# Performance work log

Hardware: AMD Instinct MI355X
Metric: run time of the kernel (lower is better)

## Reference

```python
import jax, jax.numpy as jnp
from jax import lax
import numpy as np

COMMITMENT_COST = 0.25
N_EMBED = 512
EDIM = 32


def _conv(x, w, b, stride, pad):
    # x: NCHW, w: OIHW (torch Conv2d layout)
    y = lax.conv_general_dilated(x, w, (stride, stride), [(pad, pad), (pad, pad)],
                                 dimension_numbers=("NCHW", "OIHW", "NCHW"))
    return y + b[None, :, None, None]


def _conv_t(x, w, b, stride, pad):
    # torch ConvTranspose2d weight layout: (in, out, kH, kW)
    k = w.shape[2]
    w_ = jnp.flip(w, (2, 3)).transpose(1, 0, 2, 3)  # -> OIHW
    p = k - 1 - pad
    y = lax.conv_general_dilated(x, w_, (1, 1), [(p, p), (p, p)],
                                 lhs_dilation=(stride, stride),
                                 dimension_numbers=("NCHW", "OIHW", "NCHW"))
    return y + b[None, :, None, None]


def setup_inputs() -> dict:
    key = jax.random.key(0)
    ks = jax.random.split(key, 9)
    rn = lambda k, s: jax.random.normal(k, s, jnp.float32) * 0.05
    return {
        "x": jax.random.normal(ks[0], (32, 3, 256, 256), jnp.float32),
        "e_w1": rn(ks[1], (64, 3, 4, 4)),    "e_b1": jnp.zeros((64,), jnp.float32),
        "e_w2": rn(ks[2], (128, 64, 4, 4)),  "e_b2": jnp.zeros((128,), jnp.float32),
        "e_w3": rn(ks[3], (32, 128, 3, 3)),  "e_b3": jnp.zeros((32,), jnp.float32),
        "embed": jax.random.uniform(ks[4], (N_EMBED, EDIM), jnp.float32,
                                    -1.0 / N_EMBED, 1.0 / N_EMBED),
        "d_w1": rn(ks[5], (32, 128, 3, 3)),  "d_b1": jnp.zeros((128,), jnp.float32),
        "d_w2": rn(ks[6], (128, 64, 4, 4)),  "d_b2": jnp.zeros((64,), jnp.float32),
        "d_w3": rn(ks[7], (64, 3, 4, 4)),    "d_b3": jnp.zeros((3,), jnp.float32),
    }


def reference(x, e_w1, e_b1, e_w2, e_b2, e_w3, e_b3, embed,
              d_w1, d_b1, d_w2, d_b2, d_w3, d_b3):
    # ---- encoder ----
    h = jax.nn.relu(_conv(x, e_w1, e_b1, 2, 1))   # [B,64,128,128]
    h = jax.nn.relu(_conv(h, e_w2, e_b2, 2, 1))   # [B,128,64,64]
    z = jax.nn.relu(_conv(h, e_w3, e_b3, 1, 1))   # [B,32,64,64]
    # ---- vector quantizer ----
    zp = z.transpose(0, 2, 3, 1)                  # BHWC
    zf = zp.reshape(-1, EDIM)                     # [N, 32]
    d = (zf ** 2).sum(1, keepdims=True) + (embed ** 2).sum(1) \
        - 2.0 * zf @ embed.T                      # [N, n_embed]
    idx = jnp.argmin(d, axis=1)                   # [N]
    z_q = embed[idx].reshape(zp.shape)            # gather == onehot @ embed
    sg = lax.stop_gradient
    loss = jnp.mean((sg(z_q) - zp) ** 2) + COMMITMENT_COST * jnp.mean((z_q - sg(zp)) ** 2)
    z_q_st = zp + sg(z_q - zp)                    # straight-through
    z_q_st = z_q_st.transpose(0, 3, 1, 2)         # back to NCHW
    # ---- decoder ----
    h = jax.nn.relu(_conv_t(z_q_st, d_w1, d_b1, 1, 1))  # [B,128,64,64]
    h = jax.nn.relu(_conv_t(h, d_w2, d_b2, 2, 1))       # [B,64,128,128]
    x_recon = _conv_t(h, d_w3, d_b3, 2, 1)              # [B,3,256,256]
    return x_recon, loss
```

## Files before the change

kernel.cpp:

```cpp
#include <hip/hip_runtime.h>


typedef __attribute__((ext_vector_type(8))) short     short8;
typedef __attribute__((ext_vector_type(4))) short     s16x4;
typedef __attribute__((ext_vector_type(8))) __bf16    bf16x8;
typedef __attribute__((ext_vector_type(4))) float     f32x4;
typedef __attribute__((ext_vector_type(4))) unsigned  uint32x4;

#define BATCH 32

__device__ __forceinline__ float b2f(unsigned short b) {
  union { unsigned u; float f; } v; v.u = ((unsigned)b) << 16; return v.f;
}
__device__ __forceinline__ unsigned short f2b(float f) {
  union { float f; unsigned u; } v; v.f = f;
  unsigned r = v.u + 0x7FFF + ((v.u >> 16) & 1);
  return (unsigned short)(r >> 16);
}

__global__ __launch_bounds__(256) void prep1v_k(const float* __restrict__ w,
                                                unsigned short* __restrict__ wq) {
  const int i = blockIdx.x*256 + threadIdx.x;
  const int j = i & 7, l = (i >> 3) & 63, ni = (i >> 9) & 3, ks = i >> 11;
  const int k = ks*32 + (l >> 4)*8 + j;
  const int co = ni*16 + (l & 15);
  wq[i] = (k < 48) ? f2b(w[co*48 + k]) : (unsigned short)0;
}
__global__ __launch_bounds__(256) void prep2v_k(const float* __restrict__ w,
                                                unsigned short* __restrict__ wq) {
  const int i = blockIdx.x*256 + threadIdx.x;
  const int j = i & 7, l = (i >> 3) & 63, ni = (i >> 9) & 7, ks = i >> 12;
  const int lm = l & 15, lk = l >> 4;
  const int tap = ks >> 1, cc = ks & 1;
  const int co = ni*16 + lm, ci = cc*32 + lk*8 + j;
  wq[i] = f2b(w[(co*64 + ci)*16 + tap]);
}
__global__ __launch_bounds__(256) void prep3_k(const float* __restrict__ w,
                                               unsigned short* __restrict__ wq) {
  const int i = blockIdx.x*256 + threadIdx.x;
  const int ci = i & 127, co = (i >> 7) & 31, t = i >> 12;
  wq[i] = f2b(w[(co*128 + ci)*9 + t]);
}
__global__ __launch_bounds__(256) void prep4_k(const float* __restrict__ w,
                                               unsigned short* __restrict__ wq) {
  const int i = blockIdx.x*256 + threadIdx.x;
  const int ci = i & 31, co = (i >> 5) & 127, t = i >> 12;
  wq[i] = f2b(w[(ci*128 + co)*9 + (8 - t)]);
}
__global__ __launch_bounds__(256) void prep5v_k(const float* __restrict__ w,
                                                unsigned short* __restrict__ wq) {
  const int i = blockIdx.x*256 + threadIdx.x;
  const int j = i & 7, l = (i >> 3) & 63, ni = (i >> 9) & 3;
  const int ks = (i >> 11) & 15, p = i >> 15;
  const int lm = l & 15, lk = l >> 4;
  const int py = p >> 1, px = p & 1;
  const int a = ks >> 3, b = (ks >> 2) & 1, cc = ks & 3;
  const int co = ni*16 + lm, ci = cc*32 + lk*8 + j;
  const int ky = 3 - 2*a - py, kx = 3 - 2*b - px;
  wq[i] = f2b(w[(ci*64 + co)*16 + ky*4 + kx]);
}
__global__ __launch_bounds__(256) void prep6_k(const float* __restrict__ w,
                                               unsigned short* __restrict__ wq) {
  const int i = blockIdx.x*256 + threadIdx.x;
  const int j = i & 7, l = (i >> 3) & 63, kc = (i >> 9) & 7, p = i >> 12;
  const int lm = l & 15, lk = l >> 4;
  const int a = kc >> 2, b = (kc >> 1) & 1, ch = kc & 1;
  const int ci = ch*32 + lk*8 + j, co = lm;
  const int py = p >> 1, px = p & 1;
  const int ky = 2 - 2*a + (1 - py), kx = 2 - 2*b + (1 - px);
  wq[i] = (co < 3) ? f2b(w[(ci*3 + co)*16 + ky*4 + kx]) : (unsigned short)0;
}

template<int CIN,int COUT,int HIN,int S,int KW,int NTAPS,int OSTRIDE,int P,
         bool PARITY,bool RELU,bool INF32,bool OUTF32>
__global__ __launch_bounds__(256) void mconv_k(const void* __restrict__ in_,
    const unsigned short* __restrict__ wq_, const float* __restrict__ bias,
    void* __restrict__ out_) {
  constexpr int NF  = COUT / 16;
  constexpr int NCH = CIN / 32;
  __shared__ short Al[128*40];
  __shared__ short Bl[COUT*40];
  int py = 0, px = 0, PY = P, PX = P;
  const unsigned short* wq = wq_;
  if (PARITY) {
    py = blockIdx.y >> 1; px = blockIdx.y & 1;
    PY = 1 - py; PX = 1 - px;
    wq += blockIdx.y * (NTAPS*COUT*CIN);
  }
  const int m0 = blockIdx.x * 128;
  const int w  = threadIdx.x >> 6, l = threadIdx.x & 63;
  const int lm = l & 15, lk = l >> 4;
  f32x4 acc[2][NF];
  #pragma unroll
  for (int mi = 0; mi < 2; ++mi)
    #pragma unroll
    for (int ni = 0; ni < NF; ++ni) acc[mi][ni] = (f32x4)0.0f;

  for (int tap = 0; tap < NTAPS; ++tap) {
    const int ky = tap / KW, kx = tap % KW;
    for (int ch = 0; ch < NCH; ++ch) {
      const int c0 = ch * 32;
      __syncthreads();
      for (int s = threadIdx.x; s < 512; s += 256) {
        const int row = s >> 2, part = s & 3;
        const int m = m0 + row;
        const int n = m >> 12, oy = (m >> 6) & 63, ox = m & 63;
        const int iy = oy*S - PY + ky, ix = ox*S - PX + kx;
        short8 v = (short8)(short)0;
        if (iy >= 0 && iy < HIN && ix >= 0 && ix < HIN) {
          const int base = ((n*HIN + iy)*HIN + ix)*CIN + c0 + part*8;
          if (INF32) {
            const float* pf = (const float*)in_ + base;
            const f32x4 f0 = *(const f32x4*)pf;
            const f32x4 f1 = *(const f32x4*)(pf + 4);
            #pragma unroll
            for (int j = 0; j < 4; ++j) {
              v[j]     = (short)f2b(f0[j]);
              v[j + 4] = (short)f2b(f1[j]);
            }
          } else {
            v = *(const short8*)((const unsigned short*)in_ + base);
          }
        }
        *(short8*)&Al[row*40 + part*8] = v;
      }
      for (int s = threadIdx.x; s < COUT*4; s += 256) {
        const int co = s >> 2, part = s & 3;
        *(short8*)&Bl[co*40 + part*8] =
            *(const short8*)(wq + (tap*COUT + co)*CIN + c0 + part*8);
      }
      __syncthreads();
      short8 av[2];
      #pragma unroll
      for (int mi = 0; mi < 2; ++mi)
        av[mi] = *(const short8*)&Al[(w*32 + mi*16 + lm)*40 + lk*8];
      #pragma unroll
      for (int ni = 0; ni < NF; ++ni) {
        const short8 bv = *(const short8*)&Bl[(ni*16 + lm)*40 + lk*8];
        #pragma unroll
        for (int mi = 0; mi < 2; ++mi)
          acc[mi][ni] = __builtin_amdgcn_mfma_f32_16x16x32_bf16(
              __builtin_bit_cast(bf16x8, av[mi]),
              __builtin_bit_cast(bf16x8, bv),
              acc[mi][ni], 0, 0, 0);
      }
    }
  }
  #pragma unroll
  for (int ni = 0; ni < NF; ++ni) {
    const int co = ni*16 + lm;
    const float bv = bias[co];
    #pragma unroll
    for (int mi = 0; mi < 2; ++mi) {
      #pragma unroll
      for (int r = 0; r < 4; ++r) {
        const int ml = w*32 + mi*16 + lk*4 + r;
        const int m  = m0 + ml;
        float vv = acc[mi][ni][r] + bv;
        if (RELU) vv = fmaxf(vv, 0.f);
        int off;
        if (OSTRIDE == 1) {
          off = m*COUT + co;
        } else {
          const int n = m >> 12, oy = (m >> 6) & 63, ox = m & 63;
          off = ((n*128 + oy*2 + py)*128 + ox*2 + px)*COUT + co;
        }
        if (OUTF32) ((float*)out_)[off] = vv;
        else ((unsigned short*)out_)[off] = f2b(vv);
      }
    }
  }
}

__global__ __launch_bounds__(256) void conv1m_k(const float* __restrict__ x,
    const unsigned short* __restrict__ wv, const float* __restrict__ bias,
    unsigned short* __restrict__ out) {
  __shared__ __align__(16) short RAW[12*264];
  __shared__ __align__(16) short IC[128*64];
  const int wid = ((blockIdx.x & 7) << 9) + (blockIdx.x >> 3);
  const int q = wid & 127, n = wid >> 7;
  for (int i = threadIdx.x; i < 396; i += 256)
    *(short8*)&RAW[i*8] = (short8)(short)0;
  __syncthreads();
  for (int s = threadIdx.x; s < 768; s += 256) {
    const int g = s >> 6, seg = s & 63;
    const int ci = g >> 2, ky = g & 3;
    const int iy = 2*q - 1 + ky;
    if (iy >= 0 && iy < 256) {
      const f32x4 v = *(const f32x4*)&x[((n*3 + ci)*256 + iy)*256 + seg*4];
      s16x4 sv;
      #pragma unroll
      for (int e = 0; e < 4; ++e) sv[e] = (short)f2b(v[e]);
      *(s16x4*)&RAW[g*264 + 4 + seg*4] = sv;
    }
  }
  __syncthreads();
  for (int s = threadIdx.x; s < 1024; s += 256) {
    const int kb = s & 7, ox = s >> 3;
    short8 v = (short8)(short)0;
    if (kb < 6) {
      const unsigned* u0 = (const unsigned*)&RAW[(2*kb  )*264 + 2*ox + 2];
      const unsigned* u1 = (const unsigned*)&RAW[(2*kb+1)*264 + 2*ox + 2];
      const unsigned a0 = u0[0], a1 = u0[1], a2 = u0[2];
      const unsigned b0 = u1[0], b1 = u1[1], b2 = u1[2];
      uint32x4 uv;
      uv[0] = (a0 >> 16) | (a1 << 16);
      uv[1] = (a1 >> 16) | (a2 << 16);
      uv[2] = (b0 >> 16) | (b1 << 16);
      uv[3] = (b1 >> 16) | (b2 << 16);
      v = __builtin_bit_cast(short8, uv);
    }
    const int bo = ((ox << 7) + (kb << 4)) ^ ((ox & 7) << 4);
    *(short8*)((char*)IC + bo) = v;
  }
  __syncthreads();
  const int w = threadIdx.x >> 6, l = threadIdx.x & 63;
  const int lm = l & 15, lk = l >> 4;
  f32x4 acc[2][4];
  #pragma unroll
  for (int mi = 0; mi < 2; ++mi)
    #pragma unroll
    for (int ni = 0; ni < 4; ++ni) acc[mi][ni] = (f32x4)0.0f;
  #pragma unroll
  for (int ks = 0; ks < 2; ++ks) {
    short8 bv[4];
    #pragma unroll
    for (int ni = 0; ni < 4; ++ni)
      bv[ni] = *(const short8*)(wv + (((ks*4 + ni)*64 + l) << 3));
    #pragma unroll
    for (int mi = 0; mi < 2; ++mi) {
      const int ox = w*32 + mi*16 + lm;
      const int bo = ((ox << 7) + (ks << 6) + (lk << 4)) ^ ((ox & 7) << 4);
      const short8 av = *(const short8*)((const char*)IC + bo);
      #pragma unroll
      for (int ni = 0; ni < 4; ++ni)
        acc[mi][ni] = __builtin_amdgcn_mfma_f32_16x16x32_bf16(
            __builtin_bit_cast(bf16x8, av),
            __builtin_bit_cast(bf16x8, bv[ni]),
            acc[mi][ni], 0, 0, 0);
    }
  }
  __syncthreads();
  #pragma unroll
  for (int mi = 0; mi < 2; ++mi)
    #pragma unroll
    for (int ni = 0; ni < 4; ++ni) {
      const int co = ni*16 + lm;
      const float bv = bias[co];
      #pragma unroll
      for (int r = 0; r < 4; ++r) {
        const int ox = w*32 + mi*16 + lk*4 + r;
        const int bo = ((ox << 7) + 2*co) ^ ((ox & 7) << 4);
        *(short*)((char*)IC + bo) = (short)f2b(fmaxf(acc[mi][ni][r] + bv, 0.f));
      }
    }
  __syncthreads();
  const long ob = ((long)(n*128 + q)) * 8192;
  for (int s = threadIdx.x; s < 1024; s += 256) {
    const int kb = s & 7, ox = s >> 3;
    const int bo = ((ox << 7) + (kb << 4)) ^ ((ox & 7) << 4);
    *(short8*)&out[ob + ox*64 + kb*8] = *(const short8*)((const char*)IC + bo);
  }
}

__global__ __launch_bounds__(256) void conv2m_k(const unsigned short* __restrict__ in,
    const unsigned short* __restrict__ wv, const float* __restrict__ bias,
    unsigned short* __restrict__ out) {
  __shared__ short IL[8*66*32];
  const int wid = (blockIdx.x & 7)*256 + (blockIdx.x >> 3);
  const int q = wid & 63, n = wid >> 6;
  const int w = threadIdx.x >> 6, l = threadIdx.x & 63;
  const int lm = l & 15, lk = l >> 4;
  const int Bd0 = lm*64 + lk*16;
  const unsigned short* wb = wv + w*1024 + l*8;
  f32x4 acc[4][2];
  #pragma unroll
  for (int mi = 0; mi < 4; ++mi)
    #pragma unroll
    for (int ni = 0; ni < 2; ++ni) acc[mi][ni] = (f32x4)0.0f;
  #pragma unroll
  for (int c = 0; c < 2; ++c) {
    if (c) __syncthreads();
    for (int i = threadIdx.x; i < 2112; i += 256) {
      const int part = i & 3, e = i >> 2;
      const int idx = e % 66, rp = e / 66;
      const int r = rp >> 1, p = rp & 1;
      const int iy = 2*q - 1 + r, ix = 2*idx - p;
      short8 v = (short8)(short)0;
      if (iy >= 0 && iy < 128 && ix >= 0 && ix < 128)
        v = *(const short8*)(in + (((n*128 + iy)*128 + ix)*64 + c*32 + part*8));
      *(short8*)&IL[e*32 + part*8] = v;
    }
    __syncthreads();
    #pragma unroll
    for (int t = 0; t < 16; ++t) {
      const int ky = t >> 2, kx = t & 3;
      const int p = 1 - (kx & 1), d = kx >> 1;
      const short8 bv0 = *(const short8*)(wb + (t*2 + c)*4096);
      const short8 bv1 = *(const short8*)(wb + (t*2 + c)*4096 + 512);
      const char* Ab = (const char*)IL + (Bd0 + d*64);
      const int imm0 = ((ky*2 + p)*66) << 6;
      #pragma unroll
      for (int mi = 0; mi < 4; ++mi) {
        const short8 av = *(const short8*)(Ab + imm0 + mi*1024);
        acc[mi][0] = __builtin_amdgcn_mfma_f32_16x16x32_bf16(
            __builtin_bit_cast(bf16x8, av), __builtin_bit_cast(bf16x8, bv0),
            acc[mi][0], 0, 0, 0);
        acc[mi][1] = __builtin_amdgcn_mfma_f32_16x16x32_bf16(
            __builtin_bit_cast(bf16x8, av), __builtin_bit_cast(bf16x8, bv1),
            acc[mi][1], 0, 0, 0);
      }
    }
  }
  #pragma unroll
  for (int mi = 0; mi < 4; ++mi)
    #pragma unroll
    for (int r = 0; r < 4; ++r) {
      const int ox = mi*16 + lk*4 + r;
      const int ob = ((n*64 + q)*64 + ox)*128;
      #pragma unroll
      for (int ni = 0; ni < 2; ++ni) {
        const int co = (w*2 + ni)*16 + lm;
        out[ob + co] = f2b(fmaxf(acc[mi][ni][r] + bias[co], 0.f));
      }
    }
}

__global__ __launch_bounds__(256) void convt2m_k(const unsigned short* __restrict__ in,
    const unsigned short* __restrict__ wv, const float* __restrict__ bias,
    unsigned short* __restrict__ out) {
  __shared__ short IL[3*66*64];
  const int wid = (blockIdx.x & 7)*256 + (blockIdx.x >> 3);
  const int q = wid & 63, n = wid >> 6;
  const int w = threadIdx.x >> 6, l = threadIdx.x & 63;
  const int py = w >> 1, px = w & 1;
  const int lm = l & 15, lk = l >> 4;
  int Wb[2][2];
  #pragma unroll
  for (int b = 0; b < 2; ++b) {
    const int e = lm + px + b;
    Wb[b][0] = (e << 7) + ((lk << 4) ^ ((e & 7) << 4));
    Wb[b][1] = Wb[b][0] ^ 0x40;
  }
  const int pyb = py * 8448;
  const unsigned short* wb = wv + w*32768 + l*8;
  f32x4 acc[4][4];
  #pragma unroll
  for (int mi = 0; mi < 4; ++mi)
    #pragma unroll
    for (int ni = 0; ni < 4; ++ni) acc[mi][ni] = (f32x4)0.0f;
  #pragma unroll
  for (int c = 0; c < 2; ++c) {
    if (c) __syncthreads();
    for (int i = threadIdx.x; i < 1584; i += 256) {
      const int part = i & 7, e = i >> 3;
      const int col = e % 66, r = e / 66;
      const int iy = q - 1 + r, ix = col - 1;
      short8 v = (short8)(short)0;
      if (iy >= 0 && iy < 64 && ix >= 0 && ix < 64)
        v = *(const short8*)(in + (((n*64 + iy)*64 + ix)*128 + c*64 + part*8));
      const int bo = (e << 7) + ((part << 4) ^ ((col & 7) << 4));
      *(short8*)((char*)IL + bo) = v;
    }
    __syncthreads();
    #pragma unroll
    for (int u = 0; u < 8; ++u) {
      const int a = u >> 2, b = (u >> 1) & 1, c1 = u & 1;
      const int ks = (a << 3) | (b << 2) | (2*c + c1);
      short8 bv[4];
      #pragma unroll
      for (int ni = 0; ni < 4; ++ni)
        bv[ni] = *(const short8*)(wb + ks*2048 + ni*512);
      const char* Ab = (const char*)IL + (pyb + Wb[b][c1]);
      const int imm0 = a*8448;
      #pragma unroll
      for (int mi = 0; mi < 4; ++mi) {
        const short8 av = *(const short8*)(Ab + imm0 + mi*2048);
        #pragma unroll
        for (int ni = 0; ni < 4; ++ni)
          acc[mi][ni] = __builtin_amdgcn_mfma_f32_16x16x32_bf16(
              __builtin_bit_cast(bf16x8, av),
              __builtin_bit_cast(bf16x8, bv[ni]),
              acc[mi][ni], 0, 0, 0);
      }
    }
  }
  const int oy = 2*q + py;
  #pragma unroll
  for (int mi = 0; mi < 4; ++mi)
    #pragma unroll
    for (int r = 0; r < 4; ++r) {
      const int ox = 2*(mi*16 + lk*4 + r) + px;
      const int ob = ((n*128 + oy)*128 + ox)*64;
      #pragma unroll
      for (int ni = 0; ni < 4; ++ni) {
        const int co = ni*16 + lm;
        out[ob + co] = f2b(fmaxf(acc[mi][ni][r] + bias[co], 0.f));
      }
    }
}

__global__ __launch_bounds__(256) void vqm_k(const float* __restrict__ z,
    const float* __restrict__ embed, float* __restrict__ zq,
    float* __restrict__ partial) {
  __shared__ short Be[512*40];
  __shared__ float en[512];
  __shared__ int   bidx[128];
  __shared__ float red[256];
  const int m0 = blockIdx.x * 128;
  for (int i = threadIdx.x; i < 4096; i += 256) {
    const int j = i >> 3, k0 = (i & 7) * 4;
    const f32x4 v = *(const f32x4*)&embed[j*32 + k0];
    s16x4 s;
    #pragma unroll
    for (int e = 0; e < 4; ++e) s[e] = (short)f2b(v[e]);
    *(s16x4*)&Be[j*40 + k0] = s;
  }
  __syncthreads();
  for (int j = threadIdx.x; j < 512; j += 256) {
    float s = 0.f;
    #pragma unroll
    for (int q = 0; q < 4; ++q) {
      const short8 v = *(const short8*)&Be[j*40 + q*8];
      #pragma unroll
      for (int e = 0; e < 8; ++e) {
        const float f = b2f((unsigned short)v[e]);
        s = fmaf(f, f, s);
      }
    }
    en[j] = s;
  }
  __syncthreads();
  const int w = threadIdx.x >> 6, l = threadIdx.x & 63;
  const int lm = l & 15, lk = l >> 4;
  const int rw = w * 32;
  short8 av[2];
  #pragma unroll
  for (int mi = 0; mi < 2; ++mi) {
    const float* zp = z + (long)(m0 + rw + mi*16 + lm)*32 + lk*8;
    const f32x4 f0 = *(const f32x4*)zp;
    const f32x4 f1 = *(const f32x4*)(zp + 4);
    short8 v;
    #pragma unroll
    for (int e = 0; e < 4; ++e) {
      v[e]     = (short)f2b(f0[e]);
      v[e + 4] = (short)f2b(f1[e]);
    }
    av[mi] = v;
  }
  float bd[2][4]; int bj[2][4];
  #pragma unroll
  for (int mi = 0; mi < 2; ++mi)
    #pragma unroll
    for (int r = 0; r < 4; ++r) { bd[mi][r] = 1e30f; bj[mi][r] = 0; }
  for (int nc = 0; nc < 8; ++nc) {
    f32x4 acc[2][4];
    #pragma unroll
    for (int mi = 0; mi < 2; ++mi)
      #pragma unroll
      for (int ni = 0; ni < 4; ++ni) acc[mi][ni] = (f32x4)0.0f;
    #pragma unroll
    for (int ni = 0; ni < 4; ++ni) {
      const short8 bv = *(const short8*)&Be[(nc*64 + ni*16 + lm)*40 + lk*8];
      #pragma unroll
      for (int mi = 0; mi < 2; ++mi)
        acc[mi][ni] = __builtin_amdgcn_mfma_f32_16x16x32_bf16(
            __builtin_bit_cast(bf16x8, av[mi]),
            __builtin_bit_cast(bf16x8, bv),
            acc[mi][ni], 0, 0, 0);
    }
    #pragma unroll
    for (int ni = 0; ni < 4; ++ni) {
      const int j = nc*64 + ni*16 + lm;
      const float e_n = en[j];
      #pragma unroll
      for (int mi = 0; mi < 2; ++mi)
        #pragma unroll
        for (int r = 0; r < 4; ++r) {
          const float d = fmaf(-2.f, acc[mi][ni][r], e_n);
          if (d < bd[mi][r]) { bd[mi][r] = d; bj[mi][r] = j; }
        }
    }
  }
  #pragma unroll
  for (int mi = 0; mi < 2; ++mi)
    #pragma unroll
    for (int r = 0; r < 4; ++r) {
      float d = bd[mi][r]; int j = bj[mi][r];
      #pragma unroll
      for (int off = 1; off < 16; off <<= 1) {
        const float od = __shfl_xor(d, off);
        const int   oj = __shfl_xor(j, off);
        if (od < d || (od == d && oj < j)) { d = od; j = oj; }
      }
      if (lm == 0) bidx[rw + mi*16 + lk*4 + r] = j;
    }
  __syncthreads();
  const int pl = threadIdx.x >> 1, hf = (threadIdx.x & 1) * 16;
  const int code = bidx[pl];
  const long pb = (long)(m0 + pl)*32 + hf;
  float se = 0.f;
  #pragma unroll
  for (int q = 0; q < 4; ++q) {
    const f32x4 ev = *(const f32x4*)&embed[code*32 + hf + q*4];
    const f32x4 zv = *(const f32x4*)&z[pb + q*4];
    *(f32x4*)&zq[pb + q*4] = ev;
    const f32x4 df = ev - zv;
    #pragma unroll
    for (int e = 0; e < 4; ++e) se = fmaf(df[e], df[e], se);
  }
  red[threadIdx.x] = se; __syncthreads();
  for (int s = 128; s > 0; s >>= 1) {
    if (threadIdx.x < s) red[threadIdx.x] += red[threadIdx.x + s];
    __syncthreads();
  }
  if (threadIdx.x == 0) partial[blockIdx.x] = red[0];
}

__global__ __launch_bounds__(256) void loss_k(const float* __restrict__ part,
                                              float* __restrict__ out) {
  __shared__ float red[256];
  const int t = threadIdx.x;
  float s = 0.f;
  #pragma unroll
  for (int q = 0; q < 4; ++q) s += part[t + q*256];
  red[t] = s; __syncthreads();
  for (int st = 128; st > 0; st >>= 1) {
    if (t < st) red[t] += red[t + st];
    __syncthreads();
  }
  if (t == 0) out[0] = red[0] * (1.25f / (131072.f * 32.f));
}

__global__ __launch_bounds__(256) void convt3m_k(const unsigned short* __restrict__ in,
    const unsigned short* __restrict__ wq6, const float* __restrict__ bias,
    float* __restrict__ out) {
  __shared__ short8 IL[3*8*66];
  const int h = blockIdx.x & 1, q = (blockIdx.x >> 1) & 127, n = blockIdx.x >> 8;
  for (int i = threadIdx.x; i < 1584; i += 256) {
    const int c8 = i & 7, t = i >> 3, ixl = t % 66, r = t / 66;
    const int iy = q - 1 + r, ix = h*64 - 1 + ixl;
    short8 v = (short8)(short)0;
    if (iy >= 0 && iy < 128 && ix >= 0 && ix < 128)
      v = *(const short8*)(in + (((long)(n*128 + iy)*128 + ix)*64 + c8*8));
    IL[(r*8 + c8)*66 + ixl] = v;
  }
  const int w = threadIdx.x >> 6, l = threadIdx.x & 63;
  const int py = w >> 1, px = w & 1;
  const int lm = l & 15, lk = l >> 4;
  short8 bfrag[8];
  #pragma unroll
  for (int kc = 0; kc < 8; ++kc)
    bfrag[kc] = *(const short8*)(wq6 + (((w*8 + kc)*64 + l) << 3));
  __syncthreads();
  f32x4 acc[4];
  #pragma unroll
  for (int mi = 0; mi < 4; ++mi) acc[mi] = (f32x4)0.0f;
  #pragma unroll
  for (int kc = 0; kc < 8; ++kc) {
    const int a = kc >> 2, b = (kc >> 1) & 1, ch = kc & 1;
    const int base = (((py + a)*8 + ch*4 + lk)*66) + px + b;
    #pragma unroll
    for (int mi = 0; mi < 4; ++mi) {
      const short8 av = *(const short8*)&IL[base + mi*16 + lm];
      acc[mi] = __builtin_amdgcn_mfma_f32_16x16x32_bf16(
          __builtin_bit_cast(bf16x8, av),
          __builtin_bit_cast(bf16x8, bfrag[kc]),
          acc[mi], 0, 0, 0);
    }
  }
  if (lm < 3) {
    const float bv = bias[lm];
    const int oy = 2*q + py;
    const long ob = ((long)(n*3 + lm))*65536 + oy*256;
    #pragma unroll
    for (int mi = 0; mi < 4; ++mi)
      #pragma unroll
      for (int r = 0; r < 4; ++r) {
        const int xq = mi*16 + lk*4 + r;
        out[ob + h*128 + 2*xq + px] = acc[mi][r] + bv;
      }
  }
}

extern "C" void kernel_launch(void* const* d_in, const int* in_sizes, int n_in,
                              void* d_out, int out_size, void* d_ws, size_t ws_size,
                              hipStream_t stream) {
  const float* x   = (const float*)d_in[0];
  const float* ew1 = (const float*)d_in[1];  const float* eb1 = (const float*)d_in[2];
  const float* ew2 = (const float*)d_in[3];  const float* eb2 = (const float*)d_in[4];
  const float* ew3 = (const float*)d_in[5];  const float* eb3 = (const float*)d_in[6];
  const float* emb = (const float*)d_in[7];
  const float* dw1 = (const float*)d_in[8];  const float* db1 = (const float*)d_in[9];
  const float* dw2 = (const float*)d_in[10]; const float* db2 = (const float*)d_in[11];
  const float* dw3 = (const float*)d_in[12]; const float* db3 = (const float*)d_in[13];
  float* out = (float*)d_out;

  uint8_t* w8 = (uint8_t*)d_ws;
  unsigned short* h1 = (unsigned short*)w8;
  unsigned short* h2 = (unsigned short*)(w8 + 67108864);
  float* z   = (float*)(w8 + 100663296);
  float* zq  = (float*)(w8 + 117440512);
  float* part = (float*)(w8 + 67108864);
  unsigned short* wq2 = (unsigned short*)(w8 + 117440512);
  unsigned short* wq3 = (unsigned short*)(w8 + 117440512 + 262144);
  unsigned short* wq1 = (unsigned short*)(w8 + 117440512 + 335872);
  unsigned short* wq4 = (unsigned short*)(w8 + 100663296);
  unsigned short* wq5 = (unsigned short*)(w8 + 100663296 + 73728);
  unsigned short* wq6 = (unsigned short*)(w8 + 100663296 + 335872);
  unsigned short* d1 = h2;
  unsigned short* d2 = h1;

  prep1v_k<<<dim3(16),256,0,stream>>>(ew1, wq1);
  prep2v_k<<<dim3(512),256,0,stream>>>(ew2, wq2);
  prep3_k<<<dim3(144),256,0,stream>>>(ew3, wq3);
  conv1m_k<<<dim3(4096),256,0,stream>>>(x, wq1, eb1, h1);
  conv2m_k<<<dim3(2048),256,0,stream>>>(h1, wq2, eb2, h2);
  mconv_k<128,32,64,1,3,9,1,1,false,true,false,true>
      <<<dim3(1024),256,0,stream>>>(h2, wq3, eb3, z);
  vqm_k<<<dim3(1024),256,0,stream>>>(z, emb, zq, part);
  loss_k<<<dim3(1),256,0,stream>>>(part, out + 6291456);
  prep4_k<<<dim3(144),256,0,stream>>>(dw1, wq4);
  prep5v_k<<<dim3(512),256,0,stream>>>(dw2, wq5);
  prep6_k<<<dim3(64),256,0,stream>>>(dw3, wq6);
  mconv_k<32,128,64,1,3,9,1,1,false,true,true,false>
      <<<dim3(1024),256,0,stream>>>(zq, wq4, db1, d1);
  convt2m_k<<<dim3(2048),256,0,stream>>>(d1, wq5, db2, d2);
  convt3m_k<<<dim3(8192),256,0,stream>>>(d2, wq6, db3, out);
}
```

Baseline: 391.1 us.

## Prefetch second channel half into registers during first-half MFMA compute

```diff
diff --git a/kernel.cpp b/kernel.cpp
--- a/kernel.cpp
+++ b/kernel.cpp
@@ -263,6 +263,36 @@
   }
 }
 
+#define C2_LOAD(c) \
+  _Pragma("unroll") \
+  for (int s = 0; s < 9; ++s) { \
+    st[s] = (short8)(short)0; \
+    if (goff[s] >= 0) st[s] = *(const short8*)(in + goff[s] + (c)*32); \
+  }
+#define C2_WRITE \
+  _Pragma("unroll") \
+  for (int s = 0; s < 9; ++s) \
+    if (lb[s] >= 0) *(short8*)((char*)IL + lb[s]) = st[s];
+#define C2_COMPUTE(c) \
+  _Pragma("unroll") \
+  for (int t = 0; t < 16; ++t) { \
+    const int ky = t >> 2, kx = t & 3; \
+    const int p = 1 - (kx & 1), d = kx >> 1; \
+    const short8 bv0 = *(const short8*)(wb + (t*2 + (c))*4096); \
+    const short8 bv1 = *(const short8*)(wb + (t*2 + (c))*4096 + 512); \
+    const char* Ab = (const char*)IL + (Bd0 + d*64); \
+    const int imm0 = ((ky*2 + p)*66) << 6; \
+    _Pragma("unroll") \
+    for (int mi = 0; mi < 4; ++mi) { \
+      const short8 av = *(const short8*)(Ab + imm0 + mi*1024); \
+      acc[mi][0] = __builtin_amdgcn_mfma_f32_16x16x32_bf16( \
+          __builtin_bit_cast(bf16x8, av), __builtin_bit_cast(bf16x8, bv0), \
+          acc[mi][0], 0, 0, 0); \
+      acc[mi][1] = __builtin_amdgcn_mfma_f32_16x16x32_bf16( \
+          __builtin_bit_cast(bf16x8, av), __builtin_bit_cast(bf16x8, bv1), \
+          acc[mi][1], 0, 0, 0); \
+    } \
+  }
 __global__ __launch_bounds__(256) void conv2m_k(const unsigned short* __restrict__ in,
     const unsigned short* __restrict__ wv, const float* __restrict__ bias,
     unsigned short* __restrict__ out) {
@@ -273,45 +303,32 @@
   const int lm = l & 15, lk = l >> 4;
   const int Bd0 = lm*64 + lk*16;
   const unsigned short* wb = wv + w*1024 + l*8;
+  int goff[9], lb[9];
+  #pragma unroll
+  for (int s = 0; s < 9; ++s) {
+    const int i = threadIdx.x + s*256;
+    const int part = i & 3, e = i >> 2;
+    const int idx = e % 66, rp = e / 66;
+    const int r = rp >> 1, p = rp & 1;
+    const int iy = 2*q - 1 + r, ix = 2*idx - p;
+    const bool ok = (i < 2112) && iy >= 0 && iy < 128 && ix >= 0 && ix < 128;
+    goff[s] = ok ? (((n*128 + iy)*128 + ix)*64 + part*8) : -1;
+    lb[s]   = (i < 2112) ? (e*64 + part*16) : -1;
+  }
   f32x4 acc[4][2];
   #pragma unroll
   for (int mi = 0; mi < 4; ++mi)
     #pragma unroll
     for (int ni = 0; ni < 2; ++ni) acc[mi][ni] = (f32x4)0.0f;
-  #pragma unroll
-  for (int c = 0; c < 2; ++c) {
-    if (c) __syncthreads();
-    for (int i = threadIdx.x; i < 2112; i += 256) {
-      const int part = i & 3, e = i >> 2;
-      const int idx = e % 66, rp = e / 66;
-      const int r = rp >> 1, p = rp & 1;
-      const int iy = 2*q - 1 + r, ix = 2*idx - p;
-      short8 v = (short8)(short)0;
-      if (iy >= 0 && iy < 128 && ix >= 0 && ix < 128)
-        v = *(const short8*)(in + (((n*128 + iy)*128 + ix)*64 + c*32 + part*8));
-      *(short8*)&IL[e*32 + part*8] = v;
-    }
-    __syncthreads();
-    #pragma unroll
-    for (int t = 0; t < 16; ++t) {
-      const int ky = t >> 2, kx = t & 3;
-      const int p = 1 - (kx & 1), d = kx >> 1;
-      const short8 bv0 = *(const short8*)(wb + (t*2 + c)*4096);
-      const short8 bv1 = *(const short8*)(wb + (t*2 + c)*4096 + 512);
-      const char* Ab = (const char*)IL + (Bd0 + d*64);
-      const int imm0 = ((ky*2 + p)*66) << 6;
-      #pragma unroll
-      for (int mi = 0; mi < 4; ++mi) {
-        const short8 av = *(const short8*)(Ab + imm0 + mi*1024);
-        acc[mi][0] = __builtin_amdgcn_mfma_f32_16x16x32_bf16(
-            __builtin_bit_cast(bf16x8, av), __builtin_bit_cast(bf16x8, bv0),
-            acc[mi][0], 0, 0, 0);
-        acc[mi][1] = __builtin_amdgcn_mfma_f32_16x16x32_bf16(
-            __builtin_bit_cast(bf16x8, av), __builtin_bit_cast(bf16x8, bv1),
-            acc[mi][1], 0, 0, 0);
-      }
-    }
-  }
+  short8 st[9];
+  C2_LOAD(0); C2_WRITE;
+  __syncthreads();
+  C2_LOAD(1);
+  C2_COMPUTE(0);
+  __syncthreads();
+  C2_WRITE;
+  __syncthreads();
+  C2_COMPUTE(1);
   #pragma unroll
   for (int mi = 0; mi < 4; ++mi)
     #pragma unroll
@@ -326,6 +343,38 @@
     }
 }
 
+#define CT2_LOAD(c) \
+  _Pragma("unroll") \
+  for (int s = 0; s < 7; ++s) { \
+    st[s] = (short8)(short)0; \
+    if (goff[s] >= 0) st[s] = *(const short8*)(in + goff[s] + (c)*64); \
+  }
+#define CT2_WRITE \
+  _Pragma("unroll") \
+  for (int s = 0; s < 7; ++s) \
+    if (lb[s] >= 0) *(short8*)((char*)IL + lb[s]) = st[s];
+#define CT2_COMPUTE(c) \
+  _Pragma("unroll") \
+  for (int u = 0; u < 8; ++u) { \
+    const int a = u >> 2, b = (u >> 1) & 1, c1 = u & 1; \
+    const int ks = (a << 3) | (b << 2) | (2*(c) + c1); \
+    short8 bv[4]; \
+    _Pragma("unroll") \
+    for (int ni = 0; ni < 4; ++ni) \
+      bv[ni] = *(const short8*)(wb + ks*2048 + ni*512); \
+    const char* Ab = (const char*)IL + (pyb + Wb[b][c1]); \
+    const int imm0 = a*8448; \
+    _Pragma("unroll") \
+    for (int mi = 0; mi < 4; ++mi) { \
+      const short8 av = *(const short8*)(Ab + imm0 + mi*2048); \
+      _Pragma("unroll") \
+      for (int ni = 0; ni < 4; ++ni) \
+        acc[mi][ni] = __builtin_amdgcn_mfma_f32_16x16x32_bf16( \
+            __builtin_bit_cast(bf16x8, av), \
+            __builtin_bit_cast(bf16x8, bv[ni]), \
+            acc[mi][ni], 0, 0, 0); \
+    } \
+  }
 __global__ __launch_bounds__(256) void convt2m_k(const unsigned short* __restrict__ in,
     const unsigned short* __restrict__ wv, const float* __restrict__ bias,
     unsigned short* __restrict__ out) {
@@ -344,47 +393,31 @@
   }
   const int pyb = py * 8448;
   const unsigned short* wb = wv + w*32768 + l*8;
+  int goff[7], lb[7];
+  #pragma unroll
+  for (int s = 0; s < 7; ++s) {
+    const int i = threadIdx.x + s*256;
+    const int part = i & 7, e = i >> 3;
+    const int col = e % 66, r = e / 66;
+    const int iy = q - 1 + r, ix = col - 1;
+    const bool ok = (i < 1584) && iy >= 0 && iy < 64 && ix >= 0 && ix < 64;
+    goff[s] = ok ? (((n*64 + iy)*64 + ix)*128 + part*8) : -1;
+    lb[s]   = (i < 1584) ? ((e << 7) + ((part << 4) ^ ((col & 7) << 4))) : -1;
+  }
   f32x4 acc[4][4];
   #pragma unroll
   for (int mi = 0; mi < 4; ++mi)
     #pragma unroll
     for (int ni = 0; ni < 4; ++ni) acc[mi][ni] = (f32x4)0.0f;
-  #pragma unroll
-  for (int c = 0; c < 2; ++c) {
-    if (c) __syncthreads();
-    for (int i = threadIdx.x; i < 1584; i += 256) {
-      const int part = i & 7, e = i >> 3;
-      const int col = e % 66, r = e / 66;
-      const int iy = q - 1 + r, ix = col - 1;
-      short8 v = (short8)(short)0;
-      if (iy >= 0 && iy < 64 && ix >= 0 && ix < 64)
-        v = *(const short8*)(in + (((n*64 + iy)*64 + ix)*128 + c*64 + part*8));
-      const int bo = (e << 7) + ((part << 4) ^ ((col & 7) << 4));
-      *(short8*)((char*)IL + bo) = v;
-    }
-    __syncthreads();
-    #pragma unroll
-    for (int u = 0; u < 8; ++u) {
-      const int a = u >> 2, b = (u >> 1) & 1, c1 = u & 1;
-      const int ks = (a << 3) | (b << 2) | (2*c + c1);
-      short8 bv[4];
-      #pragma unroll
-      for (int ni = 0; ni < 4; ++ni)
-        bv[ni] = *(const short8*)(wb + ks*2048 + ni*512);
-      const char* Ab = (const char*)IL + (pyb + Wb[b][c1]);
-      const int imm0 = a*8448;
-      #pragma unroll
-      for (int mi = 0; mi < 4; ++mi) {
-        const short8 av = *(const short8*)(Ab + imm0 + mi*2048);
-        #pragma unroll
-        for (int ni = 0; ni < 4; ++ni)
-          acc[mi][ni] = __builtin_amdgcn_mfma_f32_16x16x32_bf16(
-              __builtin_bit_cast(bf16x8, av),
-              __builtin_bit_cast(bf16x8, bv[ni]),
-              acc[mi][ni], 0, 0, 0);
-      }
-    }
-  }
+  short8 st[7];
+  CT2_LOAD(0); CT2_WRITE;
+  __syncthreads();
+  CT2_LOAD(1);
+  CT2_COMPUTE(0);
+  __syncthreads();
+  CT2_WRITE;
+  __syncthreads();
+  CT2_COMPUTE(1);
   const int oy = 2*q + py;
   #pragma unroll
   for (int mi = 0; mi < 4; ++mi)
```

After: 382.2 us. 2.3% less time.
